# Kernel optimization log

Hardware: AMD Instinct MI355X
Metric: run time of the kernel (lower is better)

The kernel has to match this reference:

```python
import math
import jax, jax.numpy as jnp
import numpy as np

B, N, ND, CD, H, L, T = 2, 384, 8, 16, 128, 4, 100

def silu(x):
    return x * jax.nn.sigmoid(x)

def mlp2(x, w1, b1, w2, b2):
    return silu(x @ w1 + b1) @ w2 + b2

def setup_inputs() -> dict:
    key = jax.random.key(0)
    ks = iter(jax.random.split(key, 80))
    def nrm(shape, scale=1.0):
        return jax.random.normal(next(ks), shape, jnp.float32) * scale
    def lin(fi, fo):
        s = 1.0 / np.sqrt(fi)
        return nrm((fi, fo), s), nrm((fo,), s)
    def stack_lin(fi, fo):
        ws, bs = zip(*[lin(fi, fo) for _ in range(L)])
        return jnp.stack(ws), jnp.stack(bs)
    inp = {}
    inp['node_features'] = nrm((B, N, ND))
    inp['positions'] = nrm((B, N, 2))
    inp['mask'] = jnp.ones((B, N), jnp.float32)
    inp['condition'] = nrm((B, CD))
    inp['targets'] = nrm((B, 4))
    inp['property_weights'] = jax.random.uniform(next(ks), (4,), jnp.float32)
    inp['feature_noise'] = nrm((B, N, ND))
    inp['position_noise'] = nrm((B, N, 2))
    inp['timesteps'] = jax.random.randint(next(ks), (B,), 0, T)
    inp['time_w1'], inp['time_b1'] = lin(H, H)
    inp['time_w2'], inp['time_b2'] = lin(H, H)
    inp['cond_w1'], inp['cond_b1'] = lin(CD, H)
    inp['cond_w2'], inp['cond_b2'] = lin(H, H)
    inp['nodep_w1'], inp['nodep_b1'] = lin(ND + 2, H)
    inp['nodep_w2'], inp['nodep_b2'] = lin(H, H)
    inp['edge_w1'], inp['edge_b1'] = stack_lin(2 * H + 1, H)
    inp['edge_w2'], inp['edge_b2'] = stack_lin(H, H)
    inp['nodem_w1'], inp['nodem_b1'] = stack_lin(2 * H, H)
    inp['nodem_w2'], inp['nodem_b2'] = stack_lin(H, H)
    inp['feat_w1'], inp['feat_b1'] = lin(H, H)
    inp['feat_w2'], inp['feat_b2'] = lin(H, ND)
    inp['pos_w1'], inp['pos_b1'] = lin(H, H)
    inp['pos_w2'], inp['pos_b2'] = lin(H, 2)
    inp['prop_w1'], inp['prop_b1'] = lin(H, H)
    inp['prop_w2'], inp['prop_b2'] = lin(H, H // 2)
    inp['prop_w3'], inp['prop_b3'] = lin(H // 2, 4)
    return inp

def reference(node_features, positions, mask, condition, targets, property_weights,
              feature_noise, position_noise, timesteps,
              time_w1, time_b1, time_w2, time_b2,
              cond_w1, cond_b1, cond_w2, cond_b2,
              nodep_w1, nodep_b1, nodep_w2, nodep_b2,
              edge_w1, edge_b1, edge_w2, edge_b2,
              nodem_w1, nodem_b1, nodem_w2, nodem_b2,
              feat_w1, feat_b1, feat_w2, feat_b2,
              pos_w1, pos_b1, pos_w2, pos_b2,
              prop_w1, prop_b1, prop_w2, prop_b2, prop_w3, prop_b3):
    # diffusion schedule buffers
    betas = jnp.linspace(1e-4, 0.02, T)
    alpha_bars = jnp.cumprod(1.0 - betas)
    ab = alpha_bars[timesteps][:, None, None]
    nf = jnp.sqrt(ab) * node_features + jnp.sqrt(1.0 - ab) * feature_noise
    npos = jnp.sqrt(ab) * positions + jnp.sqrt(1.0 - ab) * position_noise
    # sinusoidal time embedding
    half = H // 2
    factor = math.log(10000.0) / (half - 1)
    freqs = jnp.exp(jnp.arange(half) * (-factor))
    te = timesteps.astype(jnp.float32)[:, None] * freqs[None, :]
    temb = jnp.concatenate([jnp.sin(te), jnp.cos(te)], -1)
    state = (mlp2(jnp.concatenate([nf, npos], -1), nodep_w1, nodep_b1, nodep_w2, nodep_b2)
             + mlp2(temb, time_w1, time_b1, time_w2, time_b2)[:, None, :]
             + mlp2(condition, cond_w1, cond_b1, cond_w2, cond_b2)[:, None, :])
    # pairwise distances (fixed across layers); eps for grad-safe sqrt at diagonal
    rel = npos[:, :, None, :] - npos[:, None, :, :]
    dist = jnp.sqrt(jnp.sum(rel * rel, -1) + 1e-12)  # [B,N,N]
    emask = mask[:, :, None] * mask[:, None, :]       # [B,N,N]
    denom = jnp.clip(emask.sum(2), 1.0)[..., None]    # [B,N,1]
    mask3 = mask[..., None]

    def layer(s, p):
        ew1, eb1, ew2, eb2, nw1, nb1, nw2, nb2 = p
        # split first edge-linear: cat([node_i, node_j, dist]) @ ew1
        ai = s @ ew1[:H]            # [B,N,H] (i contribution)
        aj = s @ ew1[H:2 * H]       # [B,N,H] (j contribution)
        h = silu(ai[:, :, None, :] + aj[:, None, :, :] + dist[..., None] * ew1[2 * H] + eb1)
        msg = (h @ ew2 + eb2) * emask[..., None]
        agg = msg.sum(2) / denom    # [B,N,H]
        upd = silu(s @ nw1[:H] + agg @ nw1[H:] + nb1) @ nw2 + nb2
        return s + upd * mask3, None

    state, _ = jax.lax.scan(layer, state,
                            (edge_w1, edge_b1, edge_w2, edge_b2,
                             nodem_w1, nodem_b1, nodem_w2, nodem_b2))
    pred_fn = mlp2(state, feat_w1, feat_b1, feat_w2, feat_b2)
    pred_pn = mlp2(state, pos_w1, pos_b1, pos_w2, pos_b2)
    gemb = (state * mask3).sum(1) / jnp.clip(mask.sum(1, keepdims=True), 1.0)
    props = silu(silu(gemb @ prop_w1 + prop_b1) @ prop_w2 + prop_b2) @ prop_w3 + prop_b3
    msum = jnp.clip(mask.sum(), 1.0)
    floss = (((pred_fn - feature_noise) ** 2) * mask3).sum() / msum
    ploss = (((pred_pn - position_noise) ** 2) * mask3).sum() / msum
    noise_loss = floss + ploss
    prop_loss = (((props - targets) ** 2) * property_weights).mean()
    total_loss = noise_loss + prop_loss
    return jnp.stack([noise_loss, prop_loss, total_loss])
```

## Files before the change

kernel.cpp:

```cpp
#include <hip/hip_runtime.h>
#include <math.h>

#define BB 2
#define NN 384
#define ND 8
#define CD 16
#define HH 128
#define LL 4
#define TT 100
#define TOTN (BB * NN)

__device__ __forceinline__ float silu_f(float x) {
    float s = 1.0f / (1.0f + __expf(-x));
    return x * s;
}

__global__ void k_prep(const float* __restrict__ mask, const float* __restrict__ condition,
                       const int* __restrict__ timesteps,
                       const float* __restrict__ time_w1, const float* __restrict__ time_b1,
                       const float* __restrict__ time_w2, const float* __restrict__ time_b2,
                       const float* __restrict__ cond_w1, const float* __restrict__ cond_b1,
                       const float* __restrict__ cond_w2, const float* __restrict__ cond_b2,
                       float* __restrict__ tc, float* __restrict__ scal, float* __restrict__ accums) {
    int b = blockIdx.x;
    int t = threadIdx.x;
    __shared__ float sh[HH];
    __shared__ float sh2[HH];
    __shared__ float shc[CD];
    __shared__ float red[HH];

    if (b == 0 && t < 2) accums[t] = 0.0f;

    int ts = timesteps[b];
    float ab = 1.0f;
    for (int k = 0; k <= ts; ++k) {
        float beta = 1e-4f + (0.02f - 1e-4f) * ((float)k / (float)(TT - 1));
        ab *= (1.0f - beta);
    }
    if (t == 0) {
        scal[b * 4 + 0] = sqrtf(ab);
        scal[b * 4 + 1] = sqrtf(1.0f - ab);
    }
    float m = 0.0f;
    for (int j = t; j < NN; j += HH) m += mask[b * NN + j];
    red[t] = m;
    __syncthreads();
    for (int s = 64; s > 0; s >>= 1) {
        if (t < s) red[t] += red[t + s];
        __syncthreads();
    }
    if (t == 0) scal[b * 4 + 2] = red[0];

    const int half = HH / 2;
    float factor = logf(10000.0f) / (float)(half - 1);
    float tf = (float)ts;
    float temb;
    if (t < half) temb = sinf(tf * __expf(-factor * (float)t));
    else          temb = cosf(tf * __expf(-factor * (float)(t - half)));
    sh[t] = temb;
    if (t < CD) shc[t] = condition[b * CD + t];
    __syncthreads();

    float acc = time_b1[t];
    for (int k = 0; k < HH; ++k) acc += sh[k] * time_w1[k * HH + t];
    sh2[t] = silu_f(acc);
    __syncthreads();
    float acc2 = time_b2[t];
    for (int k = 0; k < HH; ++k) acc2 += sh2[k] * time_w2[k * HH + t];
    float acc3 = cond_b1[t];
    for (int k = 0; k < CD; ++k) acc3 += shc[k] * cond_w1[k * HH + t];
    __syncthreads();
    sh[t] = silu_f(acc3);
    __syncthreads();
    float acc4 = cond_b2[t];
    for (int k = 0; k < HH; ++k) acc4 += sh[k] * cond_w2[k * HH + t];

    tc[b * HH + t] = acc2 + acc4;
}

__global__ __launch_bounds__(256) void k_node_init(
    const float* __restrict__ node_features, const float* __restrict__ positions,
    const float* __restrict__ feature_noise, const float* __restrict__ position_noise,
    const float* __restrict__ nodep_w1, const float* __restrict__ nodep_b1,
    const float* __restrict__ nodep_w2, const float* __restrict__ nodep_b2,
    const float* __restrict__ tc, const float* __restrict__ scal,
    const float* __restrict__ ew1_0, const float* __restrict__ eb1_0,
    float* __restrict__ state, float* __restrict__ npos,
    float* __restrict__ ai0, float* __restrict__ aj0) {
    const int tid = threadIdx.x;
    const int t = tid & 127;
    const int g = tid >> 7;
    const int b0 = blockIdx.x * 4;
    const int b = b0 / NN;

    __shared__ __align__(16) float x[4][12];
    __shared__ __align__(16) float sh1[4][HH];
    __shared__ __align__(16) float sst[4][HH];
    __shared__ float sred[4][2][HH];

    if (tid < 40) {
        int n = tid / 10, c = tid % 10;
        int gn = b0 + n;
        float sab = scal[b * 4 + 0], s1ab = scal[b * 4 + 1];
        float v;
        if (c < ND) {
            v = sab * node_features[gn * ND + c] + s1ab * feature_noise[gn * ND + c];
        } else {
            int d = c - ND;
            v = sab * positions[gn * 2 + d] + s1ab * position_noise[gn * 2 + d];
            npos[gn * 2 + d] = v;
        }
        x[n][c] = v;
    }
    __syncthreads();

    for (int n = 2 * g; n <= 2 * g + 1; ++n) {
        float a = nodep_b1[t];
        #pragma unroll
        for (int k = 0; k < ND + 2; ++k) a += x[n][k] * nodep_w1[k * HH + t];
        sh1[n][t] = silu_f(a);
    }
    __syncthreads();

    {
        float a0 = 0, a1 = 0, a2 = 0, a3 = 0;
        const int k0 = g * 64;
        const float* wr = nodep_w2 + (size_t)k0 * HH + t;
        for (int kk = 0; kk < 64; kk += 4) {
            float w0 = wr[(kk + 0) * HH], w1 = wr[(kk + 1) * HH];
            float w2 = wr[(kk + 2) * HH], w3 = wr[(kk + 3) * HH];
            float4 s;
            s = *(const float4*)&sh1[0][k0 + kk]; a0 += s.x * w0 + s.y * w1 + s.z * w2 + s.w * w3;
            s = *(const float4*)&sh1[1][k0 + kk]; a1 += s.x * w0 + s.y * w1 + s.z * w2 + s.w * w3;
            s = *(const float4*)&sh1[2][k0 + kk]; a2 += s.x * w0 + s.y * w1 + s.z * w2 + s.w * w3;
            s = *(const float4*)&sh1[3][k0 + kk]; a3 += s.x * w0 + s.y * w1 + s.z * w2 + s.w * w3;
        }
        sred[0][g][t] = a0; sred[1][g][t] = a1; sred[2][g][t] = a2; sred[3][g][t] = a3;
    }
    __syncthreads();
    {
        float tcv = nodep_b2[t] + tc[b * HH + t];
        for (int n = 2 * g; n <= 2 * g + 1; ++n) {
            float st = sred[n][0][t] + sred[n][1][t] + tcv;
            state[(size_t)(b0 + n) * HH + t] = st;
            sst[n][t] = st;
        }
    }
    __syncthreads();

    {
        float a0 = 0, a1 = 0, a2 = 0, a3 = 0;
        const int k0 = g * 64;
        const float* wr = ew1_0 + (size_t)k0 * HH + t;
        for (int kk = 0; kk < 64; kk += 4) {
            float w0 = wr[(kk + 0) * HH], w1 = wr[(kk + 1) * HH];
            float w2 = wr[(kk + 2) * HH], w3 = wr[(kk + 3) * HH];
            float4 s;
            s = *(const float4*)&sst[0][k0 + kk]; a0 += s.x * w0 + s.y * w1 + s.z * w2 + s.w * w3;
            s = *(const float4*)&sst[1][k0 + kk]; a1 += s.x * w0 + s.y * w1 + s.z * w2 + s.w * w3;
            s = *(const float4*)&sst[2][k0 + kk]; a2 += s.x * w0 + s.y * w1 + s.z * w2 + s.w * w3;
            s = *(const float4*)&sst[3][k0 + kk]; a3 += s.x * w0 + s.y * w1 + s.z * w2 + s.w * w3;
        }
        sred[0][g][t] = a0; sred[1][g][t] = a1; sred[2][g][t] = a2; sred[3][g][t] = a3;
    }
    __syncthreads();
    for (int n = 2 * g; n <= 2 * g + 1; ++n)
        ai0[(size_t)(b0 + n) * HH + t] = sred[n][0][t] + sred[n][1][t] + eb1_0[t];
    __syncthreads();
    {
        float a0 = 0, a1 = 0, a2 = 0, a3 = 0;
        const int k0 = g * 64;
        const float* wr = ew1_0 + (size_t)(HH + k0) * HH + t;
        for (int kk = 0; kk < 64; kk += 4) {
            float w0 = wr[(kk + 0) * HH], w1 = wr[(kk + 1) * HH];
            float w2 = wr[(kk + 2) * HH], w3 = wr[(kk + 3) * HH];
            float4 s;
            s = *(const float4*)&sst[0][k0 + kk]; a0 += s.x * w0 + s.y * w1 + s.z * w2 + s.w * w3;
            s = *(const float4*)&sst[1][k0 + kk]; a1 += s.x * w0 + s.y * w1 + s.z * w2 + s.w * w3;
            s = *(const float4*)&sst[2][k0 + kk]; a2 += s.x * w0 + s.y * w1 + s.z * w2 + s.w * w3;
            s = *(const float4*)&sst[3][k0 + kk]; a3 += s.x * w0 + s.y * w1 + s.z * w2 + s.w * w3;
        }
        sred[0][g][t] = a0; sred[1][g][t] = a1; sred[2][g][t] = a2; sred[3][g][t] = a3;
    }
    __syncthreads();
    for (int n = 2 * g; n <= 2 * g + 1; ++n)
        aj0[(size_t)(b0 + n) * HH + t] = sred[n][0][t] + sred[n][1][t];
}

__global__ void k_dist(const float* __restrict__ npos, float* __restrict__ dist) {
    int idx = blockIdx.x * blockDim.x + threadIdx.x;
    if (idx >= BB * NN * NN) return;
    int b = idx / (NN * NN);
    int r = idx % (NN * NN);
    int i = r / NN, j = r % NN;
    float dx = npos[(b * NN + i) * 2 + 0] - npos[(b * NN + j) * 2 + 0];
    float dy = npos[(b * NN + i) * 2 + 1] - npos[(b * NN + j) * 2 + 1];
    dist[idx] = sqrtf(dx * dx + dy * dy + 1e-12f);
}

__global__ __launch_bounds__(256) void k_edge(
    const float* __restrict__ ai, const float* __restrict__ aj,
    const float* __restrict__ dist, const float* __restrict__ mask,
    const float* __restrict__ wd, float* __restrict__ Sp) {
    const int tid = threadIdx.x;
    const int t = tid & 127;
    const int g = tid >> 7;
    const int blk = blockIdx.x;
    const int p = blk >> 2, q = blk & 3;
    const int n0 = p * 2, n1 = p * 2 + 1;
    const int b = n0 / NN;
    const int jb = q * 96;

    __shared__ __align__(16) float4 sdm[96];
    __shared__ float sred[2][2][HH];

    for (int i = tid; i < 96; i += 256) {
        int j = jb + i;
        sdm[i] = make_float4(dist[(size_t)n0 * NN + j], dist[(size_t)n1 * NN + j],
                             mask[b * NN + j], 0.0f);
    }
    const float av0 = ai[(size_t)n0 * HH + t];
    const float av1 = ai[(size_t)n1 * HH + t];
    const float wdt = wd[t];
    __syncthreads();

    const float* pa = aj + ((size_t)b * NN + jb) * HH + t;
    float acc0 = 0.0f, acc1 = 0.0f;
    #pragma unroll 4
    for (int i = g; i < 96; i += 2) {
        float4 dm = sdm[i];
        float a = pa[(size_t)i * HH];
        float v0 = av0 + a + dm.x * wdt;
        float v1 = av1 + a + dm.y * wdt;
        acc0 = fmaf(dm.z, silu_f(v0), acc0);
        acc1 = fmaf(dm.z, silu_f(v1), acc1);
    }
    sred[0][g][t] = acc0;
    sred[1][g][t] = acc1;
    __syncthreads();
    if (g == 0) Sp[((size_t)q * TOTN + n0) * HH + t] = sred[0][0][t] + sred[0][1][t];
    else        Sp[((size_t)q * TOTN + n1) * HH + t] = sred[1][0][t] + sred[1][1][t];
}

template<bool LAST>
__global__ __launch_bounds__(512) void k_nodeup(
    const float* __restrict__ Sp, float* __restrict__ state,
    const float* __restrict__ mask, const float* __restrict__ scal,
    const float* __restrict__ ew2, const float* __restrict__ eb2,
    const float* __restrict__ nw1, const float* __restrict__ nb1,
    const float* __restrict__ nw2, const float* __restrict__ nb2,
    const float* __restrict__ ew1n, const float* __restrict__ eb1n,
    float* __restrict__ ai_out, float* __restrict__ aj_out,
    const float* __restrict__ fnoise, const float* __restrict__ pnoise,
    const float* __restrict__ fw1, const float* __restrict__ fb1,
    const float* __restrict__ fw2, const float* __restrict__ fb2,
    const float* __restrict__ pw1, const float* __restrict__ pb1,
    const float* __restrict__ pw2, const float* __restrict__ pb2,
    float* __restrict__ accums, float* __restrict__ gembp) {
    const int tid = threadIdx.x;
    const int t = tid & 127;
    const int g = tid >> 7;
    const int b0 = blockIdx.x * 2;
    const int b = b0 / NN;

    __shared__ __align__(16) float sS[2][HH];
    __shared__ __align__(16) float sst[2][HH];
    __shared__ __align__(16) float sagg[2][HH];
    __shared__ __align__(16) float sh[2][HH];
    __shared__ float sred[2][4][HH];
    __shared__ float lf, lp;

    if (tid < 2 * HH) {
        int n = tid >> 7, tt = tid & 127;
        int gn = b0 + n;
        sS[n][tt] = Sp[((size_t)0 * TOTN + gn) * HH + tt] + Sp[((size_t)1 * TOTN + gn) * HH + tt]
                  + Sp[((size_t)2 * TOTN + gn) * HH + tt] + Sp[((size_t)3 * TOTN + gn) * HH + tt];
        sst[n][tt] = state[(size_t)gn * HH + tt];
    }
    if (tid == 0) { lf = 0.0f; lp = 0.0f; }
    __syncthreads();

    {
        float a0 = 0, a1 = 0;
        const int k0 = g * 32;
        const float* wr = ew2 + (size_t)k0 * HH + t;
        for (int kk = 0; kk < 32; kk += 4) {
            float w0 = wr[(kk + 0) * HH], w1 = wr[(kk + 1) * HH];
            float w2 = wr[(kk + 2) * HH], w3 = wr[(kk + 3) * HH];
            float4 s;
            s = *(const float4*)&sS[0][k0 + kk]; a0 += s.x * w0 + s.y * w1 + s.z * w2 + s.w * w3;
            s = *(const float4*)&sS[1][k0 + kk]; a1 += s.x * w0 + s.y * w1 + s.z * w2 + s.w * w3;
        }
        sred[0][g][t] = a0; sred[1][g][t] = a1;
    }
    __syncthreads();
    if (g < 2) {
        const float msum = scal[b * 4 + 2];
        float mi = mask[b0 + g];
        float denom = fmaxf(mi * msum, 1.0f);
        float a = sred[g][0][t] + sred[g][1][t] + sred[g][2][t] + sred[g][3][t] + msum * eb2[t];
        sagg[g][t] = mi * a / denom;
    }
    __syncthreads();

    {
        float a0 = 0, a1 = 0;
        const int r0 = g * 64;
        const float* wr = nw1 + (size_t)r0 * HH + t;
        const float (*inp)[HH] = (g < 2) ? (const float (*)[HH])sst : (const float (*)[HH])sagg;
        const int rb = (g & 1) * 64;
        for (int kk = 0; kk < 64; kk += 4) {
            float w0 = wr[(kk + 0) * HH], w1 = wr[(kk + 1) * HH];
            float w2 = wr[(kk + 2) * HH], w3 = wr[(kk + 3) * HH];
            float4 s;
            s = *(const float4*)&inp[0][rb + kk]; a0 += s.x * w0 + s.y * w1 + s.z * w2 + s.w * w3;
            s = *(const float4*)&inp[1][rb + kk]; a1 += s.x * w0 + s.y * w1 + s.z * w2 + s.w * w3;
        }
        sred[0][g][t] = a0; sred[1][g][t] = a1;
    }
    __syncthreads();
    if (g < 2) sh[g][t] = silu_f(sred[g][0][t] + sred[g][1][t] + sred[g][2][t] + sred[g][3][t] + nb1[t]);
    __syncthreads();

    {
        float a0 = 0, a1 = 0;
        const int k0 = g * 32;
        const float* wr = nw2 + (size_t)k0 * HH + t;
        for (int kk = 0; kk < 32; kk += 4) {
            float w0 = wr[(kk + 0) * HH], w1 = wr[(kk + 1) * HH];
            float w2 = wr[(kk + 2) * HH], w3 = wr[(kk + 3) * HH];
            float4 s;
            s = *(const float4*)&sh[0][k0 + kk]; a0 += s.x * w0 + s.y * w1 + s.z * w2 + s.w * w3;
            s = *(const float4*)&sh[1][k0 + kk]; a1 += s.x * w0 + s.y * w1 + s.z * w2 + s.w * w3;
        }
        sred[0][g][t] = a0; sred[1][g][t] = a1;
    }
    __syncthreads();
    if (g < 2) {
        int gn = b0 + g;
        float mi = mask[gn];
        float ns = sst[g][t] + (sred[g][0][t] + sred[g][1][t] + sred[g][2][t] + sred[g][3][t] + nb2[t]) * mi;
        state[(size_t)gn * HH + t] = ns;
        sst[g][t] = ns;
    }
    __syncthreads();

    if (!LAST) {
        {
            float a0 = 0, a1 = 0;
            const int k0 = g * 32;
            const float* wr = ew1n + (size_t)k0 * HH + t;
            for (int kk = 0; kk < 32; kk += 4) {
                float w0 = wr[(kk + 0) * HH], w1 = wr[(kk + 1) * HH];
                float w2 = wr[(kk + 2) * HH], w3 = wr[(kk + 3) * HH];
                float4 s;
                s = *(const float4*)&sst[0][k0 + kk]; a0 += s.x * w0 + s.y * w1 + s.z * w2 + s.w * w3;
                s = *(const float4*)&sst[1][k0 + kk]; a1 += s.x * w0 + s.y * w1 + s.z * w2 + s.w * w3;
            }
            sred[0][g][t] = a0; sred[1][g][t] = a1;
        }
        __syncthreads();
        if (g < 2) ai_out[(size_t)(b0 + g) * HH + t] =
            sred[g][0][t] + sred[g][1][t] + sred[g][2][t] + sred[g][3][t] + eb1n[t];
        __syncthreads();
        {
            float a0 = 0, a1 = 0;
            const int k0 = g * 32;
            const float* wr = ew1n + (size_t)(HH + k0) * HH + t;
            for (int kk = 0; kk < 32; kk += 4) {
                float w0 = wr[(kk + 0) * HH], w1 = wr[(kk + 1) * HH];
                float w2 = wr[(kk + 2) * HH], w3 = wr[(kk + 3) * HH];
                float4 s;
                s = *(const float4*)&sst[0][k0 + kk]; a0 += s.x * w0 + s.y * w1 + s.z * w2 + s.w * w3;
                s = *(const float4*)&sst[1][k0 + kk]; a1 += s.x * w0 + s.y * w1 + s.z * w2 + s.w * w3;
            }
            sred[0][g][t] = a0; sred[1][g][t] = a1;
        }
        __syncthreads();
        if (g < 2) aj_out[(size_t)(b0 + g) * HH + t] =
            sred[g][0][t] + sred[g][1][t] + sred[g][2][t] + sred[g][3][t];
    } else {
        {
            float a0 = 0, a1 = 0;
            const int k0 = g * 32;
            const float* wr = fw1 + (size_t)k0 * HH + t;
            for (int kk = 0; kk < 32; kk += 4) {
                float w0 = wr[(kk + 0) * HH], w1 = wr[(kk + 1) * HH];
                float w2 = wr[(kk + 2) * HH], w3 = wr[(kk + 3) * HH];
                float4 s;
                s = *(const float4*)&sst[0][k0 + kk]; a0 += s.x * w0 + s.y * w1 + s.z * w2 + s.w * w3;
                s = *(const float4*)&sst[1][k0 + kk]; a1 += s.x * w0 + s.y * w1 + s.z * w2 + s.w * w3;
            }
            sred[0][g][t] = a0; sred[1][g][t] = a1;
        }
        __syncthreads();
        if (g < 2) sS[g][t] = silu_f(sred[g][0][t] + sred[g][1][t] + sred[g][2][t] + sred[g][3][t] + fb1[t]);
        __syncthreads();
        {
            float a0 = 0, a1 = 0;
            const int k0 = g * 32;
            const float* wr = pw1 + (size_t)k0 * HH + t;
            for (int kk = 0; kk < 32; kk += 4) {
                float w0 = wr[(kk + 0) * HH], w1 = wr[(kk + 1) * HH];
                float w2 = wr[(kk + 2) * HH], w3 = wr[(kk + 3) * HH];
                float4 s;
                s = *(const float4*)&sst[0][k0 + kk]; a0 += s.x * w0 + s.y * w1 + s.z * w2 + s.w * w3;
                s = *(const float4*)&sst[1][k0 + kk]; a1 += s.x * w0 + s.y * w1 + s.z * w2 + s.w * w3;
            }
            sred[0][g][t] = a0; sred[1][g][t] = a1;
        }
        __syncthreads();
        if (g < 2) sagg[g][t] = silu_f(sred[g][0][t] + sred[g][1][t] + sred[g][2][t] + sred[g][3][t] + pb1[t]);
        __syncthreads();

        if (tid < 128) {
            int n = tid >> 6, lane = tid & 63;
            int gn = b0 + n;
            float mi = mask[gn];
            if (lane < ND) {
                float o = fb2[lane];
                for (int k = 0; k < HH; ++k) o += sS[n][k] * fw2[k * ND + lane];
                float d = o - fnoise[(size_t)gn * ND + lane];
                atomicAdd(&lf, mi * d * d);
            } else if (lane < ND + 2) {
                int c = lane - ND;
                float o = pb2[c];
                for (int k = 0; k < HH; ++k) o += sagg[n][k] * pw2[k * 2 + c];
                float d = o - pnoise[(size_t)gn * 2 + c];
                atomicAdd(&lp, mi * d * d);
            }
        }
        if (g == 0) {
            float v = sst[0][t] * mask[b0] + sst[1][t] * mask[b0 + 1];
            gembp[(size_t)blockIdx.x * HH + t] = v;
        }
        __syncthreads();
        if (tid == 0) {
            atomicAdd(&accums[0], lf);
            atomicAdd(&accums[1], lp);
        }
    }
}

__global__ __launch_bounds__(256) void k_final(
    const float* __restrict__ gembp, const float* __restrict__ targets,
    const float* __restrict__ pweights,
    const float* __restrict__ w1, const float* __restrict__ b1,
    const float* __restrict__ w2, const float* __restrict__ b2,
    const float* __restrict__ w3, const float* __restrict__ b3,
    const float* __restrict__ accums, const float* __restrict__ scal,
    float* __restrict__ out) {
    const int tid = threadIdx.x;
    const int t = tid & 127;
    const int b = tid >> 7;
    __shared__ float g2[BB][HH], h1[BB][HH], h2[BB][64];
    __shared__ float pl;
    if (tid == 0) pl = 0.0f;

    float acc = 0.0f;
    const float* gp = gembp + (size_t)b * 192 * HH + t;
    #pragma unroll 8
    for (int r = 0; r < 192; ++r) acc += gp[(size_t)r * HH];
    g2[b][t] = acc / fmaxf(scal[b * 4 + 2], 1.0f);
    __syncthreads();

    float a = b1[t];
    for (int k = 0; k < HH; ++k) a += g2[b][k] * w1[k * HH + t];
    h1[b][t] = silu_f(a);
    __syncthreads();
    if (t < 64) {
        float a2 = b2[t];
        for (int k = 0; k < HH; ++k) a2 += h1[b][k] * w2[k * 64 + t];
        h2[b][t] = silu_f(a2);
    }
    __syncthreads();
    if (t < 4) {
        float o = b3[t];
        for (int k = 0; k < 64; ++k) o += h2[b][k] * w3[k * 4 + t];
        float d = o - targets[b * 4 + t];
        atomicAdd(&pl, d * d * pweights[t]);
    }
    __syncthreads();
    if (tid == 0) {
        float msumt = fmaxf(scal[0 * 4 + 2] + scal[1 * 4 + 2], 1.0f);
        float noise = (accums[0] + accums[1]) / msumt;
        float prop = pl / (float)(BB * 4);
        out[0] = noise;
        out[1] = prop;
        out[2] = noise + prop;
    }
}

extern "C" void kernel_launch(void* const* d_in, const int* in_sizes, int n_in,
                              void* d_out, int out_size, void* d_ws, size_t ws_size,
                              hipStream_t stream) {
    const float* node_features  = (const float*)d_in[0];
    const float* positions      = (const float*)d_in[1];
    const float* mask           = (const float*)d_in[2];
    const float* condition     = (const float*)d_in[3];
    const float* targets        = (const float*)d_in[4];
    const float* pweights       = (const float*)d_in[5];
    const float* feature_noise  = (const float*)d_in[6];
    const float* position_noise = (const float*)d_in[7];
    const int*   timesteps      = (const int*)d_in[8];
    const float* time_w1 = (const float*)d_in[9];
    const float* time_b1 = (const float*)d_in[10];
    const float* time_w2 = (const float*)d_in[11];
    const float* time_b2 = (const float*)d_in[12];
    const float* cond_w1 = (const float*)d_in[13];
    const float* cond_b1 = (const float*)d_in[14];
    const float* cond_w2 = (const float*)d_in[15];
    const float* cond_b2 = (const float*)d_in[16];
    const float* nodep_w1 = (const float*)d_in[17];
    const float* nodep_b1 = (const float*)d_in[18];
    const float* nodep_w2 = (const float*)d_in[19];
    const float* nodep_b2 = (const float*)d_in[20];
    const float* edge_w1 = (const float*)d_in[21];
    const float* edge_b1 = (const float*)d_in[22];
    const float* edge_w2 = (const float*)d_in[23];
    const float* edge_b2 = (const float*)d_in[24];
    const float* nodem_w1 = (const float*)d_in[25];
    const float* nodem_b1 = (const float*)d_in[26];
    const float* nodem_w2 = (const float*)d_in[27];
    const float* nodem_b2 = (const float*)d_in[28];
    const float* feat_w1 = (const float*)d_in[29];
    const float* feat_b1 = (const float*)d_in[30];
    const float* feat_w2 = (const float*)d_in[31];
    const float* feat_b2 = (const float*)d_in[32];
    const float* pos_w1 = (const float*)d_in[33];
    const float* pos_b1 = (const float*)d_in[34];
    const float* pos_w2 = (const float*)d_in[35];
    const float* pos_b2 = (const float*)d_in[36];
    const float* prop_w1 = (const float*)d_in[37];
    const float* prop_b1 = (const float*)d_in[38];
    const float* prop_w2 = (const float*)d_in[39];
    const float* prop_b2 = (const float*)d_in[40];
    const float* prop_w3 = (const float*)d_in[41];
    const float* prop_b3 = (const float*)d_in[42];

    float* ws = (float*)d_ws;
    float* npos   = ws;
    float* state  = npos + BB * NN * 2;
    float* dist   = state + TOTN * HH;
    float* aiA    = dist + (size_t)TOTN * NN;
    float* ajA    = aiA + TOTN * HH;
    float* aiB    = ajA + TOTN * HH;
    float* ajB    = aiB + TOTN * HH;
    float* Sp     = ajB + TOTN * HH;
    float* tc     = Sp + 4 * TOTN * HH;
    float* scal   = tc + BB * HH;
    float* accums = scal + BB * 4;
    float* gembp  = accums + 2;

    float* outp = (float*)d_out;

    k_prep<<<BB, HH, 0, stream>>>(mask, condition, timesteps,
                                  time_w1, time_b1, time_w2, time_b2,
                                  cond_w1, cond_b1, cond_w2, cond_b2,
                                  tc, scal, accums);
    k_node_init<<<TOTN / 4, 256, 0, stream>>>(node_features, positions, feature_noise, position_noise,
                                              nodep_w1, nodep_b1, nodep_w2, nodep_b2,
                                              tc, scal, edge_w1, edge_b1, state, npos, aiA, ajA);
    k_dist<<<(BB * NN * NN + 255) / 256, 256, 0, stream>>>(npos, dist);

    for (int l = 0; l < LL; ++l) {
        const float* ew1l = edge_w1 + (size_t)l * (2 * HH + 1) * HH;
        const float* wd   = ew1l + (size_t)(2 * HH) * HH;
        const float* ew2  = edge_w2 + (size_t)l * HH * HH;
        const float* eb2  = edge_b2 + (size_t)l * HH;
        const float* nw1  = nodem_w1 + (size_t)l * 2 * HH * HH;
        const float* nb1  = nodem_b1 + (size_t)l * HH;
        const float* nw2  = nodem_w2 + (size_t)l * HH * HH;
        const float* nb2  = nodem_b2 + (size_t)l * HH;
        const float* ew1n = edge_w1 + (size_t)(l + 1) * (2 * HH + 1) * HH;
        const float* eb1n = edge_b1 + (size_t)(l + 1) * HH;

        const float* ai_in = (l & 1) ? aiB : aiA;
        const float* aj_in = (l & 1) ? ajB : ajA;
        float* ai_out = (l & 1) ? aiA : aiB;
        float* aj_out = (l & 1) ? ajA : ajB;

        k_edge<<<TOTN / 2 * 4, 256, 0, stream>>>(ai_in, aj_in, dist, mask, wd, Sp);

        if (l < LL - 1) {
            k_nodeup<false><<<TOTN / 2, 512, 0, stream>>>(
                Sp, state, mask, scal, ew2, eb2, nw1, nb1, nw2, nb2, ew1n, eb1n,
                ai_out, aj_out,
                feature_noise, position_noise, feat_w1, feat_b1, feat_w2, feat_b2,
                pos_w1, pos_b1, pos_w2, pos_b2, accums, gembp);
        } else {
            k_nodeup<true><<<TOTN / 2, 512, 0, stream>>>(
                Sp, state, mask, scal, ew2, eb2, nw1, nb1, nw2, nb2, ew1n, eb1n,
                ai_out, aj_out,
                feature_noise, position_noise, feat_w1, feat_b1, feat_w2, feat_b2,
                pos_w1, pos_b1, pos_w2, pos_b2, accums, gembp);
        }
    }

    k_final<<<1, 256, 0, stream>>>(gembp, targets, pweights,
                                   prop_w1, prop_b1, prop_w2, prop_b2, prop_w3, prop_b3,
                                   accums, scal, outp);
}
```

Measured before the change: 320.1 us.

## Fuse edge aggregation into node-update kernel per layer

```diff
diff --git a/kernel.cpp b/kernel.cpp
--- a/kernel.cpp
+++ b/kernel.cpp
@@ -198,59 +198,17 @@
     dist[idx] = sqrtf(dx * dx + dy * dy + 1e-12f);
 }
 
-__global__ __launch_bounds__(256) void k_edge(
-    const float* __restrict__ ai, const float* __restrict__ aj,
+template<bool LAST>
+__global__ __launch_bounds__(512) void k_layer2(
+    const float* __restrict__ ai_io_in, float* __restrict__ ai_io_out,
+    const float* __restrict__ aj_in, float* __restrict__ aj_out,
     const float* __restrict__ dist, const float* __restrict__ mask,
-    const float* __restrict__ wd, float* __restrict__ Sp) {
-    const int tid = threadIdx.x;
-    const int t = tid & 127;
-    const int g = tid >> 7;
-    const int blk = blockIdx.x;
-    const int p = blk >> 2, q = blk & 3;
-    const int n0 = p * 2, n1 = p * 2 + 1;
-    const int b = n0 / NN;
-    const int jb = q * 96;
-
-    __shared__ __align__(16) float4 sdm[96];
-    __shared__ float sred[2][2][HH];
-
-    for (int i = tid; i < 96; i += 256) {
-        int j = jb + i;
-        sdm[i] = make_float4(dist[(size_t)n0 * NN + j], dist[(size_t)n1 * NN + j],
-                             mask[b * NN + j], 0.0f);
-    }
-    const float av0 = ai[(size_t)n0 * HH + t];
-    const float av1 = ai[(size_t)n1 * HH + t];
-    const float wdt = wd[t];
-    __syncthreads();
-
-    const float* pa = aj + ((size_t)b * NN + jb) * HH + t;
-    float acc0 = 0.0f, acc1 = 0.0f;
-    #pragma unroll 4
-    for (int i = g; i < 96; i += 2) {
-        float4 dm = sdm[i];
-        float a = pa[(size_t)i * HH];
-        float v0 = av0 + a + dm.x * wdt;
-        float v1 = av1 + a + dm.y * wdt;
-        acc0 = fmaf(dm.z, silu_f(v0), acc0);
-        acc1 = fmaf(dm.z, silu_f(v1), acc1);
-    }
-    sred[0][g][t] = acc0;
-    sred[1][g][t] = acc1;
-    __syncthreads();
-    if (g == 0) Sp[((size_t)q * TOTN + n0) * HH + t] = sred[0][0][t] + sred[0][1][t];
-    else        Sp[((size_t)q * TOTN + n1) * HH + t] = sred[1][0][t] + sred[1][1][t];
-}
-
-template<bool LAST>
-__global__ __launch_bounds__(512) void k_nodeup(
-    const float* __restrict__ Sp, float* __restrict__ state,
-    const float* __restrict__ mask, const float* __restrict__ scal,
+    const float* __restrict__ scal, float* __restrict__ state,
+    const float* __restrict__ wd,
     const float* __restrict__ ew2, const float* __restrict__ eb2,
     const float* __restrict__ nw1, const float* __restrict__ nb1,
     const float* __restrict__ nw2, const float* __restrict__ nb2,
     const float* __restrict__ ew1n, const float* __restrict__ eb1n,
-    float* __restrict__ ai_out, float* __restrict__ aj_out,
     const float* __restrict__ fnoise, const float* __restrict__ pnoise,
     const float* __restrict__ fw1, const float* __restrict__ fb1,
     const float* __restrict__ fw2, const float* __restrict__ fb2,
@@ -259,56 +217,82 @@
     float* __restrict__ accums, float* __restrict__ gembp) {
     const int tid = threadIdx.x;
     const int t = tid & 127;
-    const int g = tid >> 7;
-    const int b0 = blockIdx.x * 2;
-    const int b = b0 / NN;
-
-    __shared__ __align__(16) float sS[2][HH];
-    __shared__ __align__(16) float sst[2][HH];
-    __shared__ __align__(16) float sagg[2][HH];
-    __shared__ __align__(16) float sh[2][HH];
-    __shared__ float sred[2][4][HH];
+    const int q = tid >> 7;
+    const int n0 = blockIdx.x * 2;
+    const int b = n0 / NN;
+
+    __shared__ float s_d[2][NN];
+    __shared__ float s_m[NN];
+    __shared__ __align__(16) float s_S[2][HH];
+    __shared__ __align__(16) float s_st[2][HH];
+    __shared__ __align__(16) float s_agg[2][HH];
+    __shared__ __align__(16) float s_h[2][HH];
+    __shared__ float s_red[2][4][HH];
     __shared__ float lf, lp;
 
+    for (int i = tid; i < NN; i += 512) {
+        s_d[0][i] = dist[(size_t)n0 * NN + i];
+        s_d[1][i] = dist[(size_t)(n0 + 1) * NN + i];
+        s_m[i] = mask[b * NN + i];
+    }
     if (tid < 2 * HH) {
         int n = tid >> 7, tt = tid & 127;
-        int gn = b0 + n;
-        sS[n][tt] = Sp[((size_t)0 * TOTN + gn) * HH + tt] + Sp[((size_t)1 * TOTN + gn) * HH + tt]
-                  + Sp[((size_t)2 * TOTN + gn) * HH + tt] + Sp[((size_t)3 * TOTN + gn) * HH + tt];
-        sst[n][tt] = state[(size_t)gn * HH + tt];
+        s_st[n][tt] = state[(size_t)(n0 + n) * HH + tt];
     }
     if (tid == 0) { lf = 0.0f; lp = 0.0f; }
+    const float av0 = ai_io_in[(size_t)n0 * HH + t];
+    const float av1 = ai_io_in[(size_t)(n0 + 1) * HH + t];
+    const float wdt = wd[t];
+    __syncthreads();
+
+    {
+        float acc0 = 0.0f, acc1 = 0.0f;
+        const int jb = q * 96;
+        const float* pa = aj_in + ((size_t)b * NN + jb) * HH + t;
+        #pragma unroll 4
+        for (int i = 0; i < 96; ++i) {
+            float a = pa[(size_t)i * HH];
+            int j = jb + i;
+            float m = s_m[j];
+            acc0 = fmaf(m, silu_f(av0 + a + s_d[0][j] * wdt), acc0);
+            acc1 = fmaf(m, silu_f(av1 + a + s_d[1][j] * wdt), acc1);
+        }
+        s_red[0][q][t] = acc0;
+        s_red[1][q][t] = acc1;
+    }
+    __syncthreads();
+    if (q < 2) s_S[q][t] = s_red[q][0][t] + s_red[q][1][t] + s_red[q][2][t] + s_red[q][3][t];
     __syncthreads();
 
     {
         float a0 = 0, a1 = 0;
-        const int k0 = g * 32;
+        const int k0 = q * 32;
         const float* wr = ew2 + (size_t)k0 * HH + t;
         for (int kk = 0; kk < 32; kk += 4) {
             float w0 = wr[(kk + 0) * HH], w1 = wr[(kk + 1) * HH];
             float w2 = wr[(kk + 2) * HH], w3 = wr[(kk + 3) * HH];
             float4 s;
-            s = *(const float4*)&sS[0][k0 + kk]; a0 += s.x * w0 + s.y * w1 + s.z * w2 + s.w * w3;
-            s = *(const float4*)&sS[1][k0 + kk]; a1 += s.x * w0 + s.y * w1 + s.z * w2 + s.w * w3;
-        }
-        sred[0][g][t] = a0; sred[1][g][t] = a1;
-    }
-    __syncthreads();
-    if (g < 2) {
+            s = *(const float4*)&s_S[0][k0 + kk]; a0 += s.x * w0 + s.y * w1 + s.z * w2 + s.w * w3;
+            s = *(const float4*)&s_S[1][k0 + kk]; a1 += s.x * w0 + s.y * w1 + s.z * w2 + s.w * w3;
+        }
+        s_red[0][q][t] = a0; s_red[1][q][t] = a1;
+    }
+    __syncthreads();
+    if (q < 2) {
         const float msum = scal[b * 4 + 2];
-        float mi = mask[b0 + g];
+        float mi = s_m[(n0 + q) - b * NN];
         float denom = fmaxf(mi * msum, 1.0f);
-        float a = sred[g][0][t] + sred[g][1][t] + sred[g][2][t] + sred[g][3][t] + msum * eb2[t];
-        sagg[g][t] = mi * a / denom;
+        float a = s_red[q][0][t] + s_red[q][1][t] + s_red[q][2][t] + s_red[q][3][t] + msum * eb2[t];
+        s_agg[q][t] = mi * a / denom;
     }
     __syncthreads();
 
     {
         float a0 = 0, a1 = 0;
-        const int r0 = g * 64;
+        const int r0 = q * 64;
         const float* wr = nw1 + (size_t)r0 * HH + t;
-        const float (*inp)[HH] = (g < 2) ? (const float (*)[HH])sst : (const float (*)[HH])sagg;
-        const int rb = (g & 1) * 64;
+        const float (*inp)[HH] = (q < 2) ? (const float (*)[HH])s_st : (const float (*)[HH])s_agg;
+        const int rb = (q & 1) * 64;
         for (int kk = 0; kk < 64; kk += 4) {
             float w0 = wr[(kk + 0) * HH], w1 = wr[(kk + 1) * HH];
             float w2 = wr[(kk + 2) * HH], w3 = wr[(kk + 3) * HH];
@@ -316,122 +300,122 @@
             s = *(const float4*)&inp[0][rb + kk]; a0 += s.x * w0 + s.y * w1 + s.z * w2 + s.w * w3;
             s = *(const float4*)&inp[1][rb + kk]; a1 += s.x * w0 + s.y * w1 + s.z * w2 + s.w * w3;
         }
-        sred[0][g][t] = a0; sred[1][g][t] = a1;
-    }
-    __syncthreads();
-    if (g < 2) sh[g][t] = silu_f(sred[g][0][t] + sred[g][1][t] + sred[g][2][t] + sred[g][3][t] + nb1[t]);
+        s_red[0][q][t] = a0; s_red[1][q][t] = a1;
+    }
+    __syncthreads();
+    if (q < 2) s_h[q][t] = silu_f(s_red[q][0][t] + s_red[q][1][t] + s_red[q][2][t] + s_red[q][3][t] + nb1[t]);
     __syncthreads();
 
     {
         float a0 = 0, a1 = 0;
-        const int k0 = g * 32;
+        const int k0 = q * 32;
         const float* wr = nw2 + (size_t)k0 * HH + t;
         for (int kk = 0; kk < 32; kk += 4) {
             float w0 = wr[(kk + 0) * HH], w1 = wr[(kk + 1) * HH];
             float w2 = wr[(kk + 2) * HH], w3 = wr[(kk + 3) * HH];
             float4 s;
-            s = *(const float4*)&sh[0][k0 + kk]; a0 += s.x * w0 + s.y * w1 + s.z * w2 + s.w * w3;
-            s = *(const float4*)&sh[1][k0 + kk]; a1 += s.x * w0 + s.y * w1 + s.z * w2 + s.w * w3;
-        }
-        sred[0][g][t] = a0; sred[1][g][t] = a1;
-    }
-    __syncthreads();
-    if (g < 2) {
-        int gn = b0 + g;
-        float mi = mask[gn];
-        float ns = sst[g][t] + (sred[g][0][t] + sred[g][1][t] + sred[g][2][t] + sred[g][3][t] + nb2[t]) * mi;
+            s = *(const float4*)&s_h[0][k0 + kk]; a0 += s.x * w0 + s.y * w1 + s.z * w2 + s.w * w3;
+            s = *(const float4*)&s_h[1][k0 + kk]; a1 += s.x * w0 + s.y * w1 + s.z * w2 + s.w * w3;
+        }
+        s_red[0][q][t] = a0; s_red[1][q][t] = a1;
+    }
+    __syncthreads();
+    if (q < 2) {
+        int gn = n0 + q;
+        float mi = s_m[gn - b * NN];
+        float ns = s_st[q][t] + (s_red[q][0][t] + s_red[q][1][t] + s_red[q][2][t] + s_red[q][3][t] + nb2[t]) * mi;
         state[(size_t)gn * HH + t] = ns;
-        sst[g][t] = ns;
+        s_st[q][t] = ns;
     }
     __syncthreads();
 
     if (!LAST) {
         {
             float a0 = 0, a1 = 0;
-            const int k0 = g * 32;
+            const int k0 = q * 32;
             const float* wr = ew1n + (size_t)k0 * HH + t;
             for (int kk = 0; kk < 32; kk += 4) {
                 float w0 = wr[(kk + 0) * HH], w1 = wr[(kk + 1) * HH];
                 float w2 = wr[(kk + 2) * HH], w3 = wr[(kk + 3) * HH];
                 float4 s;
-                s = *(const float4*)&sst[0][k0 + kk]; a0 += s.x * w0 + s.y * w1 + s.z * w2 + s.w * w3;
-                s = *(const float4*)&sst[1][k0 + kk]; a1 += s.x * w0 + s.y * w1 + s.z * w2 + s.w * w3;
+                s = *(const float4*)&s_st[0][k0 + kk]; a0 += s.x * w0 + s.y * w1 + s.z * w2 + s.w * w3;
+                s = *(const float4*)&s_st[1][k0 + kk]; a1 += s.x * w0 + s.y * w1 + s.z * w2 + s.w * w3;
             }
-            sred[0][g][t] = a0; sred[1][g][t] = a1;
-        }
-        __syncthreads();
-        if (g < 2) ai_out[(size_t)(b0 + g) * HH + t] =
-            sred[g][0][t] + sred[g][1][t] + sred[g][2][t] + sred[g][3][t] + eb1n[t];
+            s_red[0][q][t] = a0; s_red[1][q][t] = a1;
+        }
+        __syncthreads();
+        if (q < 2) ai_io_out[(size_t)(n0 + q) * HH + t] =
+            s_red[q][0][t] + s_red[q][1][t] + s_red[q][2][t] + s_red[q][3][t] + eb1n[t];
         __syncthreads();
         {
             float a0 = 0, a1 = 0;
-            const int k0 = g * 32;
+            const int k0 = q * 32;
             const float* wr = ew1n + (size_t)(HH + k0) * HH + t;
             for (int kk = 0; kk < 32; kk += 4) {
                 float w0 = wr[(kk + 0) * HH], w1 = wr[(kk + 1) * HH];
                 float w2 = wr[(kk + 2) * HH], w3 = wr[(kk + 3) * HH];
                 float4 s;
-                s = *(const float4*)&sst[0][k0 + kk]; a0 += s.x * w0 + s.y * w1 + s.z * w2 + s.w * w3;
-                s = *(const float4*)&sst[1][k0 + kk]; a1 += s.x * w0 + s.y * w1 + s.z * w2 + s.w * w3;
+                s = *(const float4*)&s_st[0][k0 + kk]; a0 += s.x * w0 + s.y * w1 + s.z * w2 + s.w * w3;
+                s = *(const float4*)&s_st[1][k0 + kk]; a1 += s.x * w0 + s.y * w1 + s.z * w2 + s.w * w3;
             }
-            sred[0][g][t] = a0; sred[1][g][t] = a1;
-        }
-        __syncthreads();
-        if (g < 2) aj_out[(size_t)(b0 + g) * HH + t] =
-            sred[g][0][t] + sred[g][1][t] + sred[g][2][t] + sred[g][3][t];
+            s_red[0][q][t] = a0; s_red[1][q][t] = a1;
+        }
+        __syncthreads();
+        if (q < 2) aj_out[(size_t)(n0 + q) * HH + t] =
+            s_red[q][0][t] + s_red[q][1][t] + s_red[q][2][t] + s_red[q][3][t];
     } else {
         {
             float a0 = 0, a1 = 0;
-            const int k0 = g * 32;
+            const int k0 = q * 32;
             const float* wr = fw1 + (size_t)k0 * HH + t;
             for (int kk = 0; kk < 32; kk += 4) {
                 float w0 = wr[(kk + 0) * HH], w1 = wr[(kk + 1) * HH];
                 float w2 = wr[(kk + 2) * HH], w3 = wr[(kk + 3) * HH];
                 float4 s;
-                s = *(const float4*)&sst[0][k0 + kk]; a0 += s.x * w0 + s.y * w1 + s.z * w2 + s.w * w3;
-                s = *(const float4*)&sst[1][k0 + kk]; a1 += s.x * w0 + s.y * w1 + s.z * w2 + s.w * w3;
+                s = *(const float4*)&s_st[0][k0 + kk]; a0 += s.x * w0 + s.y * w1 + s.z * w2 + s.w * w3;
+                s = *(const float4*)&s_st[1][k0 + kk]; a1 += s.x * w0 + s.y * w1 + s.z * w2 + s.w * w3;
             }
-            sred[0][g][t] = a0; sred[1][g][t] = a1;
-        }
-        __syncthreads();
-        if (g < 2) sS[g][t] = silu_f(sred[g][0][t] + sred[g][1][t] + sred[g][2][t] + sred[g][3][t] + fb1[t]);
+            s_red[0][q][t] = a0; s_red[1][q][t] = a1;
+        }
+        __syncthreads();
+        if (q < 2) s_S[q][t] = silu_f(s_red[q][0][t] + s_red[q][1][t] + s_red[q][2][t] + s_red[q][3][t] + fb1[t]);
         __syncthreads();
         {
             float a0 = 0, a1 = 0;
-            const int k0 = g * 32;
+            const int k0 = q * 32;
             const float* wr = pw1 + (size_t)k0 * HH + t;
             for (int kk = 0; kk < 32; kk += 4) {
                 float w0 = wr[(kk + 0) * HH], w1 = wr[(kk + 1) * HH];
                 float w2 = wr[(kk + 2) * HH], w3 = wr[(kk + 3) * HH];
                 float4 s;
-                s = *(const float4*)&sst[0][k0 + kk]; a0 += s.x * w0 + s.y * w1 + s.z * w2 + s.w * w3;
-                s = *(const float4*)&sst[1][k0 + kk]; a1 += s.x * w0 + s.y * w1 + s.z * w2 + s.w * w3;
+                s = *(const float4*)&s_st[0][k0 + kk]; a0 += s.x * w0 + s.y * w1 + s.z * w2 + s.w * w3;
+                s = *(const float4*)&s_st[1][k0 + kk]; a1 += s.x * w0 + s.y * w1 + s.z * w2 + s.w * w3;
             }
-            sred[0][g][t] = a0; sred[1][g][t] = a1;
-        }
-        __syncthreads();
-        if (g < 2) sagg[g][t] = silu_f(sred[g][0][t] + sred[g][1][t] + sred[g][2][t] + sred[g][3][t] + pb1[t]);
+            s_red[0][q][t] = a0; s_red[1][q][t] = a1;
+        }
+        __syncthreads();
+        if (q < 2) s_agg[q][t] = silu_f(s_red[q][0][t] + s_red[q][1][t] + s_red[q][2][t] + s_red[q][3][t] + pb1[t]);
         __syncthreads();
 
         if (tid < 128) {
             int n = tid >> 6, lane = tid & 63;
-            int gn = b0 + n;
-            float mi = mask[gn];
+            int gn = n0 + n;
+            float mi = s_m[gn - b * NN];
             if (lane < ND) {
                 float o = fb2[lane];
-                for (int k = 0; k < HH; ++k) o += sS[n][k] * fw2[k * ND + lane];
+                for (int k = 0; k < HH; ++k) o += s_S[n][k] * fw2[k * ND + lane];
                 float d = o - fnoise[(size_t)gn * ND + lane];
                 atomicAdd(&lf, mi * d * d);
             } else if (lane < ND + 2) {
                 int c = lane - ND;
                 float o = pb2[c];
-                for (int k = 0; k < HH; ++k) o += sagg[n][k] * pw2[k * 2 + c];
+                for (int k = 0; k < HH; ++k) o += s_agg[n][k] * pw2[k * 2 + c];
                 float d = o - pnoise[(size_t)gn * 2 + c];
                 atomicAdd(&lp, mi * d * d);
             }
         }
-        if (g == 0) {
-            float v = sst[0][t] * mask[b0] + sst[1][t] * mask[b0 + 1];
+        if (q == 0) {
+            float v = s_st[0][t] * s_m[n0 - b * NN] + s_st[1][t] * s_m[n0 + 1 - b * NN];
             gembp[(size_t)blockIdx.x * HH + t] = v;
         }
         __syncthreads();
@@ -497,57 +481,39 @@
     const float* node_features  = (const float*)d_in[0];
     const float* positions      = (const float*)d_in[1];
     const float* mask           = (const float*)d_in[2];
-    const float* condition     = (const float*)d_in[3];
+    const float* condition      = (const float*)d_in[3];
     const float* targets        = (const float*)d_in[4];
     const float* pweights       = (const float*)d_in[5];
     const float* feature_noise  = (const float*)d_in[6];
     const float* position_noise = (const float*)d_in[7];
     const int*   timesteps      = (const int*)d_in[8];
-    const float* time_w1 = (const float*)d_in[9];
-    const float* time_b1 = (const float*)d_in[10];
-    const float* time_w2 = (const float*)d_in[11];
-    const float* time_b2 = (const float*)d_in[12];
-    const float* cond_w1 = (const float*)d_in[13];
-    const float* cond_b1 = (const float*)d_in[14];
-    const float* cond_w2 = (const float*)d_in[15];
-    const float* cond_b2 = (const float*)d_in[16];
-    const float* nodep_w1 = (const float*)d_in[17];
-    const float* nodep_b1 = (const float*)d_in[18];
-    const float* nodep_w2 = (const float*)d_in[19];
-    const float* nodep_b2 = (const float*)d_in[20];
-    const float* edge_w1 = (const float*)d_in[21];
-    const float* edge_b1 = (const float*)d_in[22];
-    const float* edge_w2 = (const float*)d_in[23];
-    const float* edge_b2 = (const float*)d_in[24];
-    const float* nodem_w1 = (const float*)d_in[25];
-    const float* nodem_b1 = (const float*)d_in[26];
-    const float* nodem_w2 = (const float*)d_in[27];
-    const float* nodem_b2 = (const float*)d_in[28];
-    const float* feat_w1 = (const float*)d_in[29];
-    const float* feat_b1 = (const float*)d_in[30];
-    const float* feat_w2 = (const float*)d_in[31];
-    const float* feat_b2 = (const float*)d_in[32];
-    const float* pos_w1 = (const float*)d_in[33];
-    const float* pos_b1 = (const float*)d_in[34];
-    const float* pos_w2 = (const float*)d_in[35];
-    const float* pos_b2 = (const float*)d_in[36];
-    const float* prop_w1 = (const float*)d_in[37];
-    const float* prop_b1 = (const float*)d_in[38];
-    const float* prop_w2 = (const float*)d_in[39];
-    const float* prop_b2 = (const float*)d_in[40];
-    const float* prop_w3 = (const float*)d_in[41];
-    const float* prop_b3 = (const float*)d_in[42];
+    const float* time_w1 = (const float*)d_in[9];   const float* time_b1 = (const float*)d_in[10];
+    const float* time_w2 = (const float*)d_in[11];  const float* time_b2 = (const float*)d_in[12];
+    const float* cond_w1 = (const float*)d_in[13];  const float* cond_b1 = (const float*)d_in[14];
+    const float* cond_w2 = (const float*)d_in[15];  const float* cond_b2 = (const float*)d_in[16];
+    const float* nodep_w1 = (const float*)d_in[17]; const float* nodep_b1 = (const float*)d_in[18];
+    const float* nodep_w2 = (const float*)d_in[19]; const float* nodep_b2 = (const float*)d_in[20];
+    const float* edge_w1 = (const float*)d_in[21];  const float* edge_b1 = (const float*)d_in[22];
+    const float* edge_w2 = (const float*)d_in[23];  const float* edge_b2 = (const float*)d_in[24];
+    const float* nodem_w1 = (const float*)d_in[25]; const float* nodem_b1 = (const float*)d_in[26];
+    const float* nodem_w2 = (const float*)d_in[27]; const float* nodem_b2 = (const float*)d_in[28];
+    const float* feat_w1 = (const float*)d_in[29];  const float* feat_b1 = (const float*)d_in[30];
+    const float* feat_w2 = (const float*)d_in[31];  const float* feat_b2 = (const float*)d_in[32];
+    const float* pos_w1 = (const float*)d_in[33];   const float* pos_b1 = (const float*)d_in[34];
+    const float* pos_w2 = (const float*)d_in[35];   const float* pos_b2 = (const float*)d_in[36];
+    const float* prop_w1 = (const float*)d_in[37];  const float* prop_b1 = (const float*)d_in[38];
+    const float* prop_w2 = (const float*)d_in[39];  const float* prop_b2 = (const float*)d_in[40];
+    const float* prop_w3 = (const float*)d_in[41];  const float* prop_b3 = (const float*)d_in[42];
 
     float* ws = (float*)d_ws;
     float* npos   = ws;
-    float* state  = npos + BB * NN * 2;
+    float* state  = npos + TOTN * 2;
     float* dist   = state + TOTN * HH;
     float* aiA    = dist + (size_t)TOTN * NN;
-    float* ajA    = aiA + TOTN * HH;
-    float* aiB    = ajA + TOTN * HH;
-    float* ajB    = aiB + TOTN * HH;
-    float* Sp     = ajB + TOTN * HH;
-    float* tc     = Sp + 4 * TOTN * HH;
+    float* aiB    = aiA + TOTN * HH;
+    float* ajA    = aiB + TOTN * HH;
+    float* ajB    = ajA + TOTN * HH;
+    float* tc     = ajB + TOTN * HH;
     float* scal   = tc + BB * HH;
     float* accums = scal + BB * 4;
     float* gembp  = accums + 2;
@@ -576,22 +542,20 @@
         const float* eb1n = edge_b1 + (size_t)(l + 1) * HH;
 
         const float* ai_in = (l & 1) ? aiB : aiA;
+        float* ai_out      = (l & 1) ? aiA : aiB;
         const float* aj_in = (l & 1) ? ajB : ajA;
-        float* ai_out = (l & 1) ? aiA : aiB;
-        float* aj_out = (l & 1) ? ajA : ajB;
-
-        k_edge<<<TOTN / 2 * 4, 256, 0, stream>>>(ai_in, aj_in, dist, mask, wd, Sp);
+        float* aj_out      = (l & 1) ? ajA : ajB;
 
         if (l < LL - 1) {
-            k_nodeup<false><<<TOTN / 2, 512, 0, stream>>>(
-                Sp, state, mask, scal, ew2, eb2, nw1, nb1, nw2, nb2, ew1n, eb1n,
-                ai_out, aj_out,
+            k_layer2<false><<<TOTN / 2, 512, 0, stream>>>(
+                ai_in, ai_out, aj_in, aj_out, dist, mask, scal, state, wd,
+                ew2, eb2, nw1, nb1, nw2, nb2, ew1n, eb1n,
                 feature_noise, position_noise, feat_w1, feat_b1, feat_w2, feat_b2,
                 pos_w1, pos_b1, pos_w2, pos_b2, accums, gembp);
         } else {
-            k_nodeup<true><<<TOTN / 2, 512, 0, stream>>>(
-                Sp, state, mask, scal, ew2, eb2, nw1, nb1, nw2, nb2, ew1n, eb1n,
-                ai_out, aj_out,
+            k_layer2<true><<<TOTN / 2, 512, 0, stream>>>(
+                ai_in, ai_out, aj_in, aj_out, dist, mask, scal, state, wd,
+                ew2, eb2, nw1, nb1, nw2, nb2, edge_w1, edge_b1,
                 feature_noise, position_noise, feat_w1, feat_b1, feat_w2, feat_b2,
                 pos_w1, pos_b1, pos_w2, pos_b2, accums, gembp);
         }
```

After: 334.1 us. 4.4% more time.
